# Kernel optimization log

Hardware: AMD Instinct MI355X
Metric: run time of the kernel (lower is better)

Reference implementation:

```python
import jax, jax.numpy as jnp
import numpy as np

B, C, H, Wd = 16, 256, 64, 64
D_MODEL = 256


def setup_inputs() -> dict:
    key = jax.random.key(0)
    kx, kw = jax.random.split(key)
    x = jax.random.normal(kx, (B, C, H, Wd), dtype=jnp.float32)
    # 1x1 conv weight [out_c=1+2*d_model, in_c], scaled like kaiming-ish init
    W = jax.random.normal(kw, (1 + 2 * D_MODEL, C), dtype=jnp.float32) / np.sqrt(C)
    return {"x": x, "W": W}


def reference(x, W):
    b, c, h, w = x.shape
    d = (W.shape[0] - 1) // 2
    n = h * w
    xf = x.reshape(b, c, n)                      # [b, c, N]
    qkv = jnp.einsum('oc,bcn->bon', W, xf)       # 1x1 conv == channel GEMM
    q = qkv[:, :1]                               # [b, 1, N]
    k = qkv[:, 1:1 + d]                          # [b, d, N]
    v = qkv[:, 1 + d:]                           # [b, d, N]
    scores = jax.nn.softmax(q, axis=-1)          # softmax over tokens
    ctx = jnp.sum(k * scores, axis=-1, keepdims=True)  # [b, d, 1]
    out = jax.nn.relu(v) * ctx                   # gated ReLU(v)
    return out.reshape(b, d, h, w)
```

## Files before the change

### kernel.cpp

```cpp
#include <hip/hip_runtime.h>
#include <cstdint>
#include <cstddef>

#define NB 16
#define NC 256
#define NN 4096
#define ND 256

typedef unsigned short u16;
typedef unsigned int u32;

typedef __attribute__((ext_vector_type(8))) short short8;
typedef __attribute__((ext_vector_type(4))) float f32x4;

__device__ __forceinline__ u16 f2bf(float f) {
  union { float f; u32 u; } v; v.f = f;
  u32 r = v.u + 0x7FFFu + ((v.u >> 16) & 1u);
  return (u16)(r >> 16);
}
__device__ __forceinline__ float bf2f(u16 h) {
  union { u32 u; float f; } v; v.u = ((u32)h) << 16; return v.f;
}

__global__ __launch_bounds__(256) void k_fuse1(const float* __restrict__ x,
                                               const float* __restrict__ W,
                                               u16* __restrict__ xbT,
                                               float* __restrict__ pm,
                                               float* __restrict__ pl,
                                               float* __restrict__ pacc) {
  __shared__ __align__(16) u16 tile[64 * 264];
  __shared__ float qred[16 * 64];
  __shared__ float qv[64];
  __shared__ float pv[64];
  const int t = threadIdx.x;
  const int b = blockIdx.y, n0 = blockIdx.x * 64;
  const float* xb = x + (size_t)b * NC * NN + n0;
  const int nl = (t & 15) * 4;
  const int cg = t >> 4;
  float q0 = 0.f, q1 = 0.f, q2 = 0.f, q3 = 0.f;
#pragma unroll
  for (int i = 0; i < 16; ++i) {
    const int c = cg + i * 16;
    float4 v = *(const float4*)(xb + (size_t)c * NN + nl);
    const float wq = W[c];
    q0 += wq * v.x; q1 += wq * v.y; q2 += wq * v.z; q3 += wq * v.w;
    tile[(nl + 0) * 264 + c] = f2bf(v.x);
    tile[(nl + 1) * 264 + c] = f2bf(v.y);
    tile[(nl + 2) * 264 + c] = f2bf(v.z);
    tile[(nl + 3) * 264 + c] = f2bf(v.w);
  }
  qred[cg * 64 + nl + 0] = q0;
  qred[cg * 64 + nl + 1] = q1;
  qred[cg * 64 + nl + 2] = q2;
  qred[cg * 64 + nl + 3] = q3;
  __syncthreads();
  if (t < 64) {
    float s = 0.f;
#pragma unroll
    for (int k = 0; k < 16; ++k) s += qred[k * 64 + t];
    qv[t] = s;
  }
  __syncthreads();
  float m = qv[0];
#pragma unroll 16
  for (int n = 1; n < 64; ++n) m = fmaxf(m, qv[n]);
  if (t < 64) pv[t] = __expf(qv[t] - m);
  __syncthreads();
  float acc = 0.f;
#pragma unroll 8
  for (int n = 0; n < 64; ++n) acc += bf2f(tile[n * 264 + t]) * pv[n];
  pacc[((size_t)b * 64 + blockIdx.x) * NC + t] = acc;
  if (t == 0) {
    float l = 0.f;
    for (int n = 0; n < 64; ++n) l += pv[n];
    pm[b * 64 + blockIdx.x] = m;
    pl[b * 64 + blockIdx.x] = l;
  }
  u16* ob = xbT + (size_t)(b * NN + n0) * NC;
#pragma unroll
  for (int i = 0; i < 8; ++i) {
    const int e = t + i * 256;
    const int rn = e >> 5;
    const int rc = (e & 31) * 8;
    *(short8*)(ob + (size_t)rn * NC + rc) = *(const short8*)&tile[rn * 264 + rc];
  }
}

__global__ __launch_bounds__(256) void k_combine(const float* __restrict__ W,
                                                 const float* __restrict__ pm,
                                                 const float* __restrict__ pl,
                                                 const float* __restrict__ pacc,
                                                 float* __restrict__ ctx,
                                                 u16* __restrict__ wvb) {
  __shared__ float sm[64], sl[64], sw[64];
  __shared__ float sx[NC];
  const int b = blockIdx.x, t = threadIdx.x;
  if (t < 64) { sm[t] = pm[b * 64 + t]; sl[t] = pl[b * 64 + t]; }
  __syncthreads();
  float M = -3.4e38f;
#pragma unroll 16
  for (int i = 0; i < 64; ++i) M = fmaxf(M, sm[i]);
  if (t < 64) sw[t] = __expf(sm[t] - M);
  __syncthreads();
  float L = 0.f;
#pragma unroll 16
  for (int i = 0; i < 64; ++i) L += sw[i] * sl[i];
  float xsc = 0.f;
#pragma unroll 8
  for (int i = 0; i < 64; ++i) xsc += sw[i] * pacc[((size_t)b * 64 + i) * NC + t];
  sx[t] = xsc / L;
  __syncthreads();
  const float* wk = W + (size_t)(1 + t) * NC;
  float a = 0.f;
#pragma unroll 4
  for (int c = 0; c < NC; ++c) a += wk[c] * sx[c];
  ctx[b * NC + t] = a;
  const float* wv = W + (size_t)(1 + ND) * NC + (size_t)b * 16 * NC;
  u16* wo = wvb + (size_t)b * 16 * NC;
#pragma unroll
  for (int i = 0; i < 16; ++i) wo[i * NC + t] = f2bf(wv[i * NC + t]);
}

#define BM 256
#define BN 128
#define BK 64

__global__ __launch_bounds__(512) void k_gemm(const u16* __restrict__ xbT,
                                              const u16* __restrict__ wvb,
                                              const float* __restrict__ ctx,
                                              float* __restrict__ out) {
  __shared__ __align__(16) u16 As[BM * BK];
  __shared__ __align__(16) u16 Bs[BN * BK];
  const int t = threadIdx.x;
  const int b = blockIdx.y;
  const int n0 = blockIdx.x * BN;
  const int lane = t & 63, w = t >> 6;
  const int wd = (w >> 1) * 64, wn = (w & 1) * 64;
  const int quad = lane >> 4, l15 = lane & 15;

  f32x4 acc[4][4];
#pragma unroll
  for (int mi = 0; mi < 4; ++mi)
#pragma unroll
    for (int ni = 0; ni < 4; ++ni)
      acc[mi][ni] = (f32x4){0.f, 0.f, 0.f, 0.f};

  const int rstg = t >> 3;
  const int l8 = ((t & 7) ^ (rstg & 7)) * 8;
  const u16* gA = wvb + (size_t)rstg * NC + l8;
  const u16* gB = xbT + (size_t)(b * NN + n0 + rstg) * NC + l8;
  const int ldst = 8 * t;

  const int pq0 = ((0 * 4 + quad) ^ (l15 & 7)) * 8;
  const int pq1 = ((1 * 4 + quad) ^ (l15 & 7)) * 8;

  for (int kk = 0; kk < NC; kk += BK) {
    __syncthreads();
#pragma unroll
    for (int i = 0; i < 4; ++i)
      __builtin_amdgcn_global_load_lds(
          (const __attribute__((address_space(1))) u32*)(gA + kk + (size_t)(64 * i) * NC),
          (__attribute__((address_space(3))) u32*)(As + 4096 * i + ldst), 16, 0, 0);
#pragma unroll
    for (int i = 0; i < 2; ++i)
      __builtin_amdgcn_global_load_lds(
          (const __attribute__((address_space(1))) u32*)(gB + kk + (size_t)(64 * i) * NC),
          (__attribute__((address_space(3))) u32*)(Bs + 4096 * i + ldst), 16, 0, 0);
    __syncthreads();

#pragma unroll
    for (int kq = 0; kq < 2; ++kq) {
      const int pq = kq ? pq1 : pq0;
      short8 af[4], bfr[4];
#pragma unroll
      for (int mi = 0; mi < 4; ++mi)
        af[mi] = *(const short8*)&As[(wd + mi * 16 + l15) * BK + pq];
#pragma unroll
      for (int ni = 0; ni < 4; ++ni)
        bfr[ni] = *(const short8*)&Bs[(wn + ni * 16 + l15) * BK + pq];
#pragma unroll
      for (int mi = 0; mi < 4; ++mi)
#pragma unroll
        for (int ni = 0; ni < 4; ++ni)
          acc[mi][ni] = __builtin_amdgcn_mfma_f32_16x16x32_bf16(af[mi], bfr[ni],
                                                                acc[mi][ni], 0, 0, 0);
    }
  }

#pragma unroll
  for (int mi = 0; mi < 4; ++mi) {
#pragma unroll
    for (int r = 0; r < 4; ++r) {
      const int d = wd + mi * 16 + quad * 4 + r;
      const float cx = ctx[b * NC + d];
      float* op = out + (size_t)(b * NC + d) * NN + n0 + wn + l15;
#pragma unroll
      for (int ni = 0; ni < 4; ++ni) {
        float v = acc[mi][ni][r];
        op[ni * 16] = fmaxf(v, 0.f) * cx;
      }
    }
  }
}

extern "C" void kernel_launch(void* const* d_in, const int* in_sizes, int n_in,
                              void* d_out, int out_size, void* d_ws, size_t ws_size,
                              hipStream_t stream) {
  const float* x = (const float*)d_in[0];
  const float* W = (const float*)d_in[1];
  float* out = (float*)d_out;

  char* ws = (char*)d_ws;
  u16* xbT    = (u16*)ws;
  float* pacc = (float*)(ws + 33554432);
  float* pm   = (float*)(ws + 34603008);
  float* pl   = (float*)(ws + 34607104);
  float* ctx  = (float*)(ws + 34611200);
  u16* wvb    = (u16*)(ws + 34627584);

  k_fuse1<<<dim3(64, 16), 256, 0, stream>>>(x, W, xbT, pm, pl, pacc);
  k_combine<<<16, 256, 0, stream>>>(W, pm, pl, pacc, ctx, wvb);
  k_gemm<<<dim3(32, 16), 512, 0, stream>>>(xbT, wvb, ctx, out);
}
```

Baseline: 149.6 us.

## Restructure fused pass to transpose in registers and reduce softmax with shuffles

The first kernel now has each thread load 4x4 blocks of channels by tokens, transpose and convert them to bf16 in registers, and write 8-byte chunks straight to the transposed global buffer. This removes the large LDS staging tile, which needed scattered 2-byte stores. The query max and sum reductions now use wavefront shuffles. The weighted channel sums are built from register partials and reduced through a padded LDS buffer. The global transposed stores are only 8 bytes wide with stride NC, which may coalesce worse than the previous 16-byte row writes.

Measured after the change: 150.7 us. About the same (+0.7%).

```diff
diff --git a/kernel.cpp b/kernel.cpp
--- a/kernel.cpp
+++ b/kernel.cpp
@@ -28,61 +28,93 @@
                                                float* __restrict__ pm,
                                                float* __restrict__ pl,
                                                float* __restrict__ pacc) {
-  __shared__ __align__(16) u16 tile[64 * 264];
-  __shared__ float qred[16 * 64];
-  __shared__ float qv[64];
-  __shared__ float pv[64];
+  __shared__ float qred[16 * 65];
+  __shared__ __align__(16) float pv[64];
+  __shared__ float pracc[16 * 257];
   const int t = threadIdx.x;
   const int b = blockIdx.y, n0 = blockIdx.x * 64;
   const float* xb = x + (size_t)b * NC * NN + n0;
   const int nl = (t & 15) * 4;
+  const int cq4 = (t >> 4) * 4;
+
+  ushort4 pk[4][4];
+  float qp0 = 0.f, qp1 = 0.f, qp2 = 0.f, qp3 = 0.f;
+
+#pragma unroll
+  for (int i = 0; i < 4; ++i) {
+    const int c0 = cq4 + 64 * i;
+    const float* xr = xb + (size_t)c0 * NN + nl;
+    float4 v0 = *(const float4*)(xr);
+    float4 v1 = *(const float4*)(xr + NN);
+    float4 v2 = *(const float4*)(xr + 2 * NN);
+    float4 v3 = *(const float4*)(xr + 3 * NN);
+    const float4 Wq = *(const float4*)(W + c0);
+    qp0 += Wq.x * v0.x + Wq.y * v1.x + Wq.z * v2.x + Wq.w * v3.x;
+    qp1 += Wq.x * v0.y + Wq.y * v1.y + Wq.z * v2.y + Wq.w * v3.y;
+    qp2 += Wq.x * v0.z + Wq.y * v1.z + Wq.z * v2.z + Wq.w * v3.z;
+    qp3 += Wq.x * v0.w + Wq.y * v1.w + Wq.z * v2.w + Wq.w * v3.w;
+    ushort4 u0 = {f2bf(v0.x), f2bf(v1.x), f2bf(v2.x), f2bf(v3.x)};
+    ushort4 u1 = {f2bf(v0.y), f2bf(v1.y), f2bf(v2.y), f2bf(v3.y)};
+    ushort4 u2 = {f2bf(v0.z), f2bf(v1.z), f2bf(v2.z), f2bf(v3.z)};
+    ushort4 u3 = {f2bf(v0.w), f2bf(v1.w), f2bf(v2.w), f2bf(v3.w)};
+    u16* ob = xbT + (size_t)(b * NN + n0 + nl) * NC + c0;
+    *(ushort4*)(ob) = u0;
+    *(ushort4*)(ob + NC) = u1;
+    *(ushort4*)(ob + 2 * NC) = u2;
+    *(ushort4*)(ob + 3 * NC) = u3;
+    pk[i][0] = u0; pk[i][1] = u1; pk[i][2] = u2; pk[i][3] = u3;
+  }
+
   const int cg = t >> 4;
-  float q0 = 0.f, q1 = 0.f, q2 = 0.f, q3 = 0.f;
-#pragma unroll
-  for (int i = 0; i < 16; ++i) {
-    const int c = cg + i * 16;
-    float4 v = *(const float4*)(xb + (size_t)c * NN + nl);
-    const float wq = W[c];
-    q0 += wq * v.x; q1 += wq * v.y; q2 += wq * v.z; q3 += wq * v.w;
-    tile[(nl + 0) * 264 + c] = f2bf(v.x);
-    tile[(nl + 1) * 264 + c] = f2bf(v.y);
-    tile[(nl + 2) * 264 + c] = f2bf(v.z);
-    tile[(nl + 3) * 264 + c] = f2bf(v.w);
-  }
-  qred[cg * 64 + nl + 0] = q0;
-  qred[cg * 64 + nl + 1] = q1;
-  qred[cg * 64 + nl + 2] = q2;
-  qred[cg * 64 + nl + 3] = q3;
-  __syncthreads();
-  if (t < 64) {
-    float s = 0.f;
-#pragma unroll
-    for (int k = 0; k < 16; ++k) s += qred[k * 64 + t];
-    qv[t] = s;
-  }
-  __syncthreads();
-  float m = qv[0];
-#pragma unroll 16
-  for (int n = 1; n < 64; ++n) m = fmaxf(m, qv[n]);
-  if (t < 64) pv[t] = __expf(qv[t] - m);
-  __syncthreads();
-  float acc = 0.f;
-#pragma unroll 8
-  for (int n = 0; n < 64; ++n) acc += bf2f(tile[n * 264 + t]) * pv[n];
-  pacc[((size_t)b * 64 + blockIdx.x) * NC + t] = acc;
+  qred[cg * 65 + nl + 0] = qp0;
+  qred[cg * 65 + nl + 1] = qp1;
+  qred[cg * 65 + nl + 2] = qp2;
+  qred[cg * 65 + nl + 3] = qp3;
+  __syncthreads();
+
+  float q = 0.f;
+#pragma unroll
+  for (int k = 0; k < 16; ++k) q += qred[k * 65 + (t & 63)];
+  float m = q;
+#pragma unroll
+  for (int off = 1; off < 64; off <<= 1) m = fmaxf(m, __shfl_xor(m, off));
+  const float p = __expf(q - m);
+  if (t < 64) pv[t] = p;
+  float l = p;
+#pragma unroll
+  for (int off = 1; off < 64; off <<= 1) l += __shfl_xor(l, off);
+  __syncthreads();
+
+  const float4 pwv = *(const float4*)&pv[nl];
+  float sc[4][4];
+#pragma unroll
+  for (int i = 0; i < 4; ++i) {
+    sc[i][0] = sc[i][1] = sc[i][2] = sc[i][3] = 0.f;
+#pragma unroll
+    for (int jn = 0; jn < 4; ++jn) {
+      const ushort4 u = pk[i][jn];
+      const float w = (jn == 0) ? pwv.x : (jn == 1) ? pwv.y : (jn == 2) ? pwv.z : pwv.w;
+      sc[i][0] += bf2f(u.x) * w;
+      sc[i][1] += bf2f(u.y) * w;
+      sc[i][2] += bf2f(u.z) * w;
+      sc[i][3] += bf2f(u.w) * w;
+    }
+  }
+#pragma unroll
+  for (int i = 0; i < 4; ++i) {
+#pragma unroll
+    for (int j = 0; j < 4; ++j)
+      pracc[(t & 15) * 257 + cq4 + 64 * i + j] = sc[i][j];
+  }
+  __syncthreads();
+
+  float xsp = 0.f;
+#pragma unroll
+  for (int k = 0; k < 16; ++k) xsp += pracc[k * 257 + t];
+  pacc[((size_t)b * 64 + blockIdx.x) * NC + t] = xsp;
   if (t == 0) {
-    float l = 0.f;
-    for (int n = 0; n < 64; ++n) l += pv[n];
     pm[b * 64 + blockIdx.x] = m;
     pl[b * 64 + blockIdx.x] = l;
-  }
-  u16* ob = xbT + (size_t)(b * NN + n0) * NC;
-#pragma unroll
-  for (int i = 0; i < 8; ++i) {
-    const int e = t + i * 256;
-    const int rn = e >> 5;
-    const int rc = (e & 31) * 8;
-    *(short8*)(ob + (size_t)rn * NC + rc) = *(const short8*)&tile[rn * 264 + rc];
   }
 }
 
```

## Transpose x in registers in fuse kernel, drop LDS tile, move Wv conversion

Applied to the files above, without the earlier changes.

The first kernel now has each thread load an 8x8 channel-by-token block, pack the bf16 transpose in registers and write it straight to the transposed buffer. This removes the 33 KB LDS tile and its scattered 2-byte stores. The softmax partial sums and per-channel weighted sums are now computed with wave shuffles instead of an LDS pass. The Wv-to-bf16 conversion moves from the combine kernel into a few blocks of the first kernel, and the combine kernel's k-projection dot product now uses float4 loads. The cost is higher register use, and only 8 blocks take on the extra conversion work.

After: 150.5 us. About the same (+0.6%).

```diff
diff --git a/kernel.cpp b/kernel.cpp
--- a/kernel.cpp
+++ b/kernel.cpp
@@ -25,64 +25,108 @@
 __global__ __launch_bounds__(256) void k_fuse1(const float* __restrict__ x,
                                                const float* __restrict__ W,
                                                u16* __restrict__ xbT,
+                                               u16* __restrict__ wvb,
                                                float* __restrict__ pm,
                                                float* __restrict__ pl,
                                                float* __restrict__ pacc) {
-  __shared__ __align__(16) u16 tile[64 * 264];
-  __shared__ float qred[16 * 64];
-  __shared__ float qv[64];
-  __shared__ float pv[64];
+  __shared__ float qred[32 * 65];
+  __shared__ float qred2[4 * 65];
   const int t = threadIdx.x;
   const int b = blockIdx.y, n0 = blockIdx.x * 64;
+  const int tx = t & 7, ty = t >> 3;
+  const int c0 = ty * 8, nl = tx * 8;
   const float* xb = x + (size_t)b * NC * NN + n0;
-  const int nl = (t & 15) * 4;
-  const int cg = t >> 4;
-  float q0 = 0.f, q1 = 0.f, q2 = 0.f, q3 = 0.f;
-#pragma unroll
-  for (int i = 0; i < 16; ++i) {
-    const int c = cg + i * 16;
-    float4 v = *(const float4*)(xb + (size_t)c * NN + nl);
-    const float wq = W[c];
-    q0 += wq * v.x; q1 += wq * v.y; q2 += wq * v.z; q3 += wq * v.w;
-    tile[(nl + 0) * 264 + c] = f2bf(v.x);
-    tile[(nl + 1) * 264 + c] = f2bf(v.y);
-    tile[(nl + 2) * 264 + c] = f2bf(v.z);
-    tile[(nl + 3) * 264 + c] = f2bf(v.w);
-  }
-  qred[cg * 64 + nl + 0] = q0;
-  qred[cg * 64 + nl + 1] = q1;
-  qred[cg * 64 + nl + 2] = q2;
-  qred[cg * 64 + nl + 3] = q3;
-  __syncthreads();
-  if (t < 64) {
+
+  const float4 w0 = *(const float4*)(W + c0);
+  const float4 w1 = *(const float4*)(W + c0 + 4);
+  const float wq[8] = {w0.x, w0.y, w0.z, w0.w, w1.x, w1.y, w1.z, w1.w};
+
+  short8 pk[8];
+  float qp[8] = {0.f, 0.f, 0.f, 0.f, 0.f, 0.f, 0.f, 0.f};
+
+#pragma unroll
+  for (int r = 0; r < 8; ++r) {
+    const float* xr = xb + (size_t)(c0 + r) * NN + nl;
+    const float4 va = *(const float4*)(xr);
+    const float4 vb = *(const float4*)(xr + 4);
+    qp[0] += wq[r] * va.x; qp[1] += wq[r] * va.y;
+    qp[2] += wq[r] * va.z; qp[3] += wq[r] * va.w;
+    qp[4] += wq[r] * vb.x; qp[5] += wq[r] * vb.y;
+    qp[6] += wq[r] * vb.z; qp[7] += wq[r] * vb.w;
+    pk[0][r] = (short)f2bf(va.x); pk[1][r] = (short)f2bf(va.y);
+    pk[2][r] = (short)f2bf(va.z); pk[3][r] = (short)f2bf(va.w);
+    pk[4][r] = (short)f2bf(vb.x); pk[5][r] = (short)f2bf(vb.y);
+    pk[6][r] = (short)f2bf(vb.z); pk[7][r] = (short)f2bf(vb.w);
+  }
+
+  u16* ob = xbT + (size_t)(b * NN + n0 + nl) * NC + c0;
+#pragma unroll
+  for (int j = 0; j < 8; ++j)
+    *(short8*)(ob + (size_t)j * NC) = pk[j];
+
+#pragma unroll
+  for (int j = 0; j < 8; ++j) qred[ty * 65 + nl + j] = qp[j];
+  __syncthreads();
+  {
+    const int n = t & 63, g = t >> 6;
     float s = 0.f;
 #pragma unroll
-    for (int k = 0; k < 16; ++k) s += qred[k * 64 + t];
-    qv[t] = s;
-  }
-  __syncthreads();
-  float m = qv[0];
-#pragma unroll 16
-  for (int n = 1; n < 64; ++n) m = fmaxf(m, qv[n]);
-  if (t < 64) pv[t] = __expf(qv[t] - m);
-  __syncthreads();
-  float acc = 0.f;
-#pragma unroll 8
-  for (int n = 0; n < 64; ++n) acc += bf2f(tile[n * 264 + t]) * pv[n];
-  pacc[((size_t)b * 64 + blockIdx.x) * NC + t] = acc;
+    for (int k = 0; k < 8; ++k) s += qred[(g * 8 + k) * 65 + n];
+    qred2[g * 65 + n] = s;
+  }
+  __syncthreads();
+
+  float q[8];
+#pragma unroll
+  for (int j = 0; j < 8; ++j)
+    q[j] = qred2[0 * 65 + nl + j] + qred2[1 * 65 + nl + j] +
+           qred2[2 * 65 + nl + j] + qred2[3 * 65 + nl + j];
+
+  float m = q[0];
+#pragma unroll
+  for (int j = 1; j < 8; ++j) m = fmaxf(m, q[j]);
+#pragma unroll
+  for (int off = 1; off < 8; off <<= 1) m = fmaxf(m, __shfl_xor(m, off));
+
+  float p[8]; float l = 0.f;
+#pragma unroll
+  for (int j = 0; j < 8; ++j) { p[j] = __expf(q[j] - m); l += p[j]; }
+#pragma unroll
+  for (int off = 1; off < 8; off <<= 1) l += __shfl_xor(l, off);
+
+  float sc[8];
+#pragma unroll
+  for (int r = 0; r < 8; ++r) {
+    float s = 0.f;
+#pragma unroll
+    for (int j = 0; j < 8; ++j) s += bf2f((u16)pk[j][r]) * p[j];
+    sc[r] = s;
+  }
+#pragma unroll
+  for (int off = 1; off < 8; off <<= 1) {
+#pragma unroll
+    for (int r = 0; r < 8; ++r) sc[r] += __shfl_xor(sc[r], off);
+  }
+  if (tx == 0) {
+    float* pp = pacc + ((size_t)b * 64 + blockIdx.x) * NC + c0;
+#pragma unroll
+    for (int r = 0; r < 8; ++r) pp[r] = sc[r];
+  }
   if (t == 0) {
-    float l = 0.f;
-    for (int n = 0; n < 64; ++n) l += pv[n];
     pm[b * 64 + blockIdx.x] = m;
     pl[b * 64 + blockIdx.x] = l;
   }
-  u16* ob = xbT + (size_t)(b * NN + n0) * NC;
-#pragma unroll
-  for (int i = 0; i < 8; ++i) {
-    const int e = t + i * 256;
-    const int rn = e >> 5;
-    const int rc = (e & 31) * 8;
-    *(short8*)(ob + (size_t)rn * NC + rc) = *(const short8*)&tile[rn * 264 + rc];
+
+  if (b == 0 && blockIdx.x < 8) {
+    const float* wv = W + (size_t)(1 + ND) * NC;
+    const int base = blockIdx.x * 8192;
+#pragma unroll
+    for (int i = 0; i < 8; ++i) {
+      const int idx = base + i * 1024 + t * 4;
+      const float4 v = *(const float4*)(wv + idx);
+      ushort4 o = {f2bf(v.x), f2bf(v.y), f2bf(v.z), f2bf(v.w)};
+      *(ushort4*)(wvb + idx) = o;
+    }
   }
 }
 
@@ -90,10 +134,9 @@
                                                  const float* __restrict__ pm,
                                                  const float* __restrict__ pl,
                                                  const float* __restrict__ pacc,
-                                                 float* __restrict__ ctx,
-                                                 u16* __restrict__ wvb) {
+                                                 float* __restrict__ ctx) {
   __shared__ float sm[64], sl[64], sw[64];
-  __shared__ float sx[NC];
+  __shared__ __align__(16) float sx[NC];
   const int b = blockIdx.x, t = threadIdx.x;
   if (t < 64) { sm[t] = pm[b * 64 + t]; sl[t] = pl[b * 64 + t]; }
   __syncthreads();
@@ -113,12 +156,12 @@
   const float* wk = W + (size_t)(1 + t) * NC;
   float a = 0.f;
 #pragma unroll 4
-  for (int c = 0; c < NC; ++c) a += wk[c] * sx[c];
+  for (int c4 = 0; c4 < 64; ++c4) {
+    const float4 w4 = *(const float4*)(wk + c4 * 4);
+    const float4 s4 = *(const float4*)&sx[c4 * 4];
+    a += w4.x * s4.x + w4.y * s4.y + w4.z * s4.z + w4.w * s4.w;
+  }
   ctx[b * NC + t] = a;
-  const float* wv = W + (size_t)(1 + ND) * NC + (size_t)b * 16 * NC;
-  u16* wo = wvb + (size_t)b * 16 * NC;
-#pragma unroll
-  for (int i = 0; i < 16; ++i) wo[i * NC + t] = f2bf(wv[i * NC + t]);
 }
 
 #define BM 256
@@ -218,7 +261,7 @@
   float* ctx  = (float*)(ws + 34611200);
   u16* wvb    = (u16*)(ws + 34627584);
 
-  k_fuse1<<<dim3(64, 16), 256, 0, stream>>>(x, W, xbT, pm, pl, pacc);
-  k_combine<<<16, 256, 0, stream>>>(W, pm, pl, pacc, ctx, wvb);
+  k_fuse1<<<dim3(64, 16), 256, 0, stream>>>(x, W, xbT, wvb, pm, pl, pacc);
+  k_combine<<<16, 256, 0, stream>>>(W, pm, pl, pacc, ctx);
   k_gemm<<<dim3(32, 16), 512, 0, stream>>>(xbT, wvb, ctx, out);
 }
```
